# Performance work log

Measured on AMD Instinct MI355X. Metric: run time of the kernel, lower is better.

## Reference

```python
import jax, jax.numpy as jnp
import numpy as np

DIM = 256; WS = 8; HEADS = 8; HD = DIM // HEADS; SCALE = HD ** -0.5; MLP_HIDDEN = 1024
B = 8; H = 128; W = 128


def setup_inputs() -> dict:
    key = jax.random.key(0)
    ks = jax.random.split(key, 16)
    def nrm(k, shape, s=0.02):
        return jax.random.normal(k, shape, jnp.float32) * s
    # relative position index (same construction as torch buffer)
    coords = np.stack(np.meshgrid(np.arange(WS), np.arange(WS), indexing='ij')).reshape(2, -1)
    rel = (coords[:, :, None] - coords[:, None, :]).transpose(1, 2, 0).astype(np.int64)
    rel[..., 0] += WS - 1; rel[..., 1] += WS - 1; rel[..., 0] *= 2 * WS - 1
    rel_idx = jnp.asarray(rel.sum(-1), jnp.int32)  # (64,64) in [0,225)
    return dict(
        x=nrm(ks[0], (B, H, W, DIM), 1.0),
        rel_table=nrm(ks[1], ((2 * WS - 1) ** 2, HEADS)),
        qkv_w=nrm(ks[2], (3 * DIM, DIM)), qkv_b=nrm(ks[3], (3 * DIM,)),
        qkv2_w=nrm(ks[4], (3 * DIM, DIM)), qkv2_b=nrm(ks[5], (3 * DIM,)),
        proj_ln_w=jnp.ones((DIM,), jnp.float32), proj_ln_b=jnp.zeros((DIM,), jnp.float32),
        proj_w=nrm(ks[6], (DIM, DIM)), proj_b=nrm(ks[7], (DIM,)),
        proj2_ln_w=jnp.ones((DIM,), jnp.float32), proj2_ln_b=jnp.zeros((DIM,), jnp.float32),
        proj2_w=nrm(ks[8], (DIM, DIM)), proj2_b=nrm(ks[9], (DIM,)),
        norm1_w=jnp.ones((DIM,), jnp.float32), norm1_b=jnp.zeros((DIM,), jnp.float32),
        norm2_w=jnp.ones((DIM,), jnp.float32), norm2_b=jnp.zeros((DIM,), jnp.float32),
        fc1_w=nrm(ks[10], (MLP_HIDDEN, DIM)), fc1_b=nrm(ks[11], (MLP_HIDDEN,)),
        fc2_w=nrm(ks[12], (DIM, MLP_HIDDEN)), fc2_b=nrm(ks[13], (DIM,)),
        rel_idx=rel_idx,
    )


def _ln(x, w, b):
    mu = x.mean(-1, keepdims=True)
    var = ((x - mu) ** 2).mean(-1, keepdims=True)
    return (x - mu) / jnp.sqrt(var + 1e-5) * w + b


def _mha(tokens, wqkv, bqkv, bias=None):
    Bt, N, C = tokens.shape
    qkv = (tokens @ wqkv.T + bqkv).reshape(Bt, N, 3, HEADS, HD).transpose(2, 0, 3, 1, 4)
    q, k, v = qkv[0] * SCALE, qkv[1], qkv[2]
    attn = jnp.einsum('bhnd,bhmd->bhnm', q, k)
    if bias is not None:
        attn = attn + bias  # (1,heads,N,N) relative position bias
    attn = jax.nn.softmax(attn, axis=-1)
    out = jnp.einsum('bhnm,bhmd->bhnd', attn, v)
    return out.transpose(0, 2, 1, 3).reshape(Bt, N, C)


def _pos_sine(h, w, c):
    # PositionEmbeddingSine(normalize=True), mask all-zero -> cumsum = 1..h / 1..w
    npf = c // 2
    scale = 2.0 * np.pi; eps = 1e-5
    y = jnp.arange(1, h + 1, dtype=jnp.float32); y = y / (y[-1] + eps) * scale
    xw = jnp.arange(1, w + 1, dtype=jnp.float32); xw = xw / (xw[-1] + eps) * scale
    dim_t = 10000.0 ** ((2.0 * (jnp.arange(npf) // 2)) / npf)
    def enc(e):  # (L,) -> (L,npf) interleaved sin/cos
        p = e[:, None] / dim_t
        return jnp.stack([jnp.sin(p[:, 0::2]), jnp.cos(p[:, 1::2])], axis=-1).reshape(e.shape[0], npf)
    py = enc(y); px = enc(xw)
    return jnp.concatenate([jnp.broadcast_to(py[:, None, :], (h, w, npf)),
                            jnp.broadcast_to(px[None, :, :], (h, w, npf))], axis=-1)  # (h,w,c)


def _upsample_ac(x, oh, ow):
    # bilinear, align_corners=True; x: (B,h,w,C)
    Bn, h, w, C = x.shape
    def idx(n, o):
        s = jnp.linspace(0.0, n - 1.0, o)
        i0 = jnp.floor(s).astype(jnp.int32)
        i1 = jnp.minimum(i0 + 1, n - 1)
        return i0, i1, s - i0
    y0, y1, ty = idx(h, oh)
    x = x[:, y0] * (1 - ty)[None, :, None, None] + x[:, y1] * ty[None, :, None, None]
    x0, x1, tx = idx(w, ow)
    x = x[:, :, x0] * (1 - tx)[None, None, :, None] + x[:, :, x1] * tx[None, None, :, None]
    return x


def reference(x, rel_table, qkv_w, qkv_b, qkv2_w, qkv2_b,
              proj_ln_w, proj_ln_b, proj_w, proj_b,
              proj2_ln_w, proj2_ln_b, proj2_w, proj2_b,
              norm1_w, norm1_b, norm2_w, norm2_b,
              fc1_w, fc1_b, fc2_w, fc2_b, rel_idx):
    Bn, Hh, Ww, C = x.shape  # H,W divisible by WS -> padding is a no-op
    nh, nw = Hh // WS, Ww // WS
    N = WS * WS
    shortcut = x
    # window partition -> (B*nh*nw, N, C)
    xw = x.reshape(Bn, nh, WS, nw, WS, C).transpose(0, 1, 3, 2, 4, 5).reshape(-1, N, C)
    bias = rel_table[rel_idx.reshape(-1)].reshape(N, N, HEADS).transpose(2, 0, 1)[None]
    xw = _mha(xw, qkv_w, qkv_b, bias)
    xw = xw.reshape(Bn, nh, nw, WS, WS, C).transpose(0, 1, 3, 2, 4, 5).reshape(Bn, Hh, Ww, C)
    x = shortcut + xw
    x = x + (_ln(x, proj_ln_w, proj_ln_b) @ proj_w.T + proj_b)
    shortcut = x
    # global branch: avgpool each window, sine pos enc, full attention, bilinear upsample
    xg = x.reshape(Bn, nh, WS, nw, WS, C).mean(axis=(2, 4))  # (B,nh,nw,C)
    xg = xg + _pos_sine(nh, nw, C)[None]
    xg = _mha(xg.reshape(Bn, nh * nw, C), qkv2_w, qkv2_b).reshape(Bn, nh, nw, C)
    xg = _upsample_ac(xg, Hh, Ww)
    x = shortcut + xg
    x = x + (_ln(x, proj2_ln_w, proj2_ln_b) @ proj2_w.T + proj2_b)
    h = _ln(x, norm1_w, norm1_b)
    h = jax.nn.gelu(h @ fc1_w.T + fc1_b, approximate=False) @ fc2_w.T + fc2_b
    x = x + h
    return _ln(x, norm2_w, norm2_b)
```

## Files before the change

### kernel.cpp

```cpp
#include <hip/hip_runtime.h>
#include <math.h>

#define DEV __device__ __forceinline__

constexpr int NTOK = 131072;
constexpr int TOKS_PER_B = 16384;
constexpr float SCALE_F = 0.17677669529663687f;

typedef float f32x4 __attribute__((ext_vector_type(4)));
typedef _Float16 half8 __attribute__((ext_vector_type(8)));
typedef _Float16 half2v __attribute__((ext_vector_type(2)));
typedef unsigned short us8 __attribute__((ext_vector_type(8)));

#if defined(__has_builtin)
#if __has_builtin(__builtin_amdgcn_fdot2)
#define HAS_FDOT2 1
#endif
#endif

DEV float gelu1(float v) { return 0.5f * v * (1.f + erff(v * 0.7071067811865476f)); }
DEV unsigned short f2h(float x) { _Float16 h = (_Float16)x; return __builtin_bit_cast(unsigned short, h); }
DEV float h2f(unsigned short u) { return (float)__builtin_bit_cast(_Float16, u); }

DEV float dot2acc(unsigned qp, unsigned kp, float acc) {
#ifdef HAS_FDOT2
  return __builtin_amdgcn_fdot2(__builtin_bit_cast(half2v, qp),
                                __builtin_bit_cast(half2v, kp), acc, false);
#else
  return acc + h2f((unsigned short)(qp & 0xffff)) * h2f((unsigned short)(kp & 0xffff))
             + h2f((unsigned short)(qp >> 16)) * h2f((unsigned short)(kp >> 16));
#endif
}

DEV int swz_row(int p) { return ((p >> 2) & ~1) | (((p >> 2) ^ (p >> 4)) & 1); }
DEV int swz_gran(int p) {
  return ((p ^ (p >> 2) ^ (p >> 4)) & 1) | ((((p >> 1) ^ (p >> 3)) & 1) << 1);
}

#define GLOAD16(src, dst)                                                        \
  __builtin_amdgcn_global_load_lds(                                              \
      (const __attribute__((address_space(1))) void*)(src),                      \
      (__attribute__((address_space(3))) void*)(dst), 16, 0, 0)

__global__ void cvtw16_k(const float* __restrict__ w, unsigned short* __restrict__ dst, int n) {
  const int i = (blockIdx.x * 256 + threadIdx.x) * 4;
  float4 v = *(const float4*)(w + i);
  ushort4 h, l;
  h.x = f2h(v.x); l.x = f2h(v.x - h2f(h.x));
  h.y = f2h(v.y); l.y = f2h(v.y - h2f(h.y));
  h.z = f2h(v.z); l.z = f2h(v.z - h2f(h.z));
  h.w = f2h(v.w); l.w = f2h(v.w - h2f(h.w));
  *(ushort4*)(dst + i) = h;
  *(ushort4*)(dst + n + i) = l;
}

__global__ void biasprep_k(const float* __restrict__ rel_table, const int* __restrict__ rel_idx,
                           float* __restrict__ biasT) {
  const int i = blockIdx.x * 256 + threadIdx.x;
  const int h = i >> 12, mr = i & 4095, m = mr >> 6, r = mr & 63;
  biasT[i] = rel_table[rel_idx[r * 64 + m] * 8 + h];
}

template <int AMODE, bool RES, bool GELU, bool OUTH, bool STATS, bool FINLN>
__launch_bounds__(256)
__global__ void gemm16(const void* __restrict__ Ain, const unsigned short* __restrict__ Wp,
                       const float* __restrict__ bias, void* __restrict__ outv,
                       const float* __restrict__ stats,
                       const float* __restrict__ lnw, const float* __restrict__ lnb,
                       float* __restrict__ statsOut,
                       const float* __restrict__ fw, const float* __restrict__ fb,
                       int M, int N, int K) {
  __shared__ __align__(16) char Asm[64 * 64];
  __shared__ __align__(16) char Wsm[2 * 256 * 64];
  const int t = threadIdx.x;
  const int lane = t & 63, wid = t >> 6;
  const int m0 = blockIdx.y * 64, n0 = blockIdx.x * 256;
  const unsigned short* Wlp = Wp + (size_t)N * K;

  f32x4 acc[4][4];
#pragma unroll
  for (int i = 0; i < 4; ++i)
#pragma unroll
    for (int j = 0; j < 4; ++j) acc[i][j] = (f32x4){0.f, 0.f, 0.f, 0.f};

  const int fr = lane & 15, G = lane >> 4;
  const int sw16 = (((4 * fr + G) ^ (fr & 7)) << 4);

  const float* Afrow = nullptr;
  const unsigned short* Ahrow = nullptr;
  int aG = 0;
  float mu = 0.f, rsg = 1.f;
  if constexpr (AMODE == 2) {
    const int p = wid * 64 + lane;
    Ahrow = (const unsigned short*)Ain + (size_t)(m0 + swz_row(p)) * K + swz_gran(p) * 8;
  } else {
    const int p = t;
    const int aR = swz_row(p);
    aG = swz_gran(p);
    Afrow = (const float*)Ain + (size_t)(m0 + aR) * K + aG * 8;
    if constexpr (AMODE == 1) {
      mu = stats[(size_t)(m0 + aR) * 2];
      rsg = stats[(size_t)(m0 + aR) * 2 + 1];
    }
  }
  const unsigned short* wsrc[8];
  int wdst[8];
#pragma unroll
  for (int j = 0; j < 8; ++j) {
    const int plane = j >> 2;
    const int bs = (wid * 4 + (j & 3)) * 64;
    const int p = bs + lane;
    wsrc[j] = (plane ? Wlp : Wp) + (size_t)(n0 + swz_row(p)) * K + swz_gran(p) * 8;
    wdst[j] = plane * (256 * 64) + bs * 16;
  }

  for (int k0 = 0; k0 < K; k0 += 32) {
#pragma unroll
    for (int j = 0; j < 8; ++j) GLOAD16(wsrc[j] + k0, Wsm + wdst[j]);
    if constexpr (AMODE == 2) {
      GLOAD16(Ahrow + k0, Asm + wid * 1024);
    } else {
      float4 v0 = *(const float4*)(Afrow + k0);
      float4 v1 = *(const float4*)(Afrow + k0 + 4);
      if constexpr (AMODE == 1) {
        const int kc = k0 + aG * 8;
        float4 w0 = *(const float4*)(lnw + kc), w1 = *(const float4*)(lnw + kc + 4);
        float4 b0 = *(const float4*)(lnb + kc), b1 = *(const float4*)(lnb + kc + 4);
        v0.x = (v0.x - mu) * rsg * w0.x + b0.x;  v0.y = (v0.y - mu) * rsg * w0.y + b0.y;
        v0.z = (v0.z - mu) * rsg * w0.z + b0.z;  v0.w = (v0.w - mu) * rsg * w0.w + b0.w;
        v1.x = (v1.x - mu) * rsg * w1.x + b1.x;  v1.y = (v1.y - mu) * rsg * w1.y + b1.y;
        v1.z = (v1.z - mu) * rsg * w1.z + b1.z;  v1.w = (v1.w - mu) * rsg * w1.w + b1.w;
      }
      us8 hh;
      hh[0] = f2h(v0.x); hh[1] = f2h(v0.y); hh[2] = f2h(v0.z); hh[3] = f2h(v0.w);
      hh[4] = f2h(v1.x); hh[5] = f2h(v1.y); hh[6] = f2h(v1.z); hh[7] = f2h(v1.w);
      *(us8*)(Asm + t * 16) = hh;
    }
    __syncthreads();
    half8 a4[4], bh4[4], bl4[4];
#pragma unroll
    for (int i = 0; i < 4; ++i) {
      a4[i] = __builtin_bit_cast(half8, *(const us8*)(Asm + i * 1024 + sw16));
      bh4[i] = __builtin_bit_cast(half8, *(const us8*)(Wsm + wid * 4096 + i * 1024 + sw16));
      bl4[i] = __builtin_bit_cast(half8,
               *(const us8*)(Wsm + 256 * 64 + wid * 4096 + i * 1024 + sw16));
    }
#pragma unroll
    for (int i = 0; i < 4; ++i)
#pragma unroll
      for (int j = 0; j < 4; ++j) {
        acc[i][j] = __builtin_amdgcn_mfma_f32_16x16x32_f16(a4[i], bh4[j], acc[i][j], 0, 0, 0);
        acc[i][j] = __builtin_amdgcn_mfma_f32_16x16x32_f16(a4[i], bl4[j], acc[i][j], 0, 0, 0);
      }
    __syncthreads();
  }
  const int g4 = (lane >> 4) * 4;
#pragma unroll
  for (int i = 0; i < 4; ++i)
#pragma unroll
    for (int j = 0; j < 4; ++j) {
      const int col = n0 + wid * 64 + j * 16 + fr;
      const float bb = bias[col];
#pragma unroll
      for (int r4 = 0; r4 < 4; ++r4) {
        const int row = m0 + i * 16 + g4 + r4;
        float v = acc[i][j][r4] + bb;
        if (GELU) v = gelu1(v);
        if (RES) v += ((const float*)outv)[(size_t)row * N + col];
        acc[i][j][r4] = v;
      }
    }
  if (STATS || FINLN) {
    __shared__ float rsum[4][64], rsq[4][64];
    float ps[4][4], pq[4][4];
#pragma unroll
    for (int i = 0; i < 4; ++i)
#pragma unroll
      for (int r4 = 0; r4 < 4; ++r4) {
        ps[i][r4] = acc[i][0][r4] + acc[i][1][r4] + acc[i][2][r4] + acc[i][3][r4];
        pq[i][r4] = acc[i][0][r4] * acc[i][0][r4] + acc[i][1][r4] * acc[i][1][r4] +
                    acc[i][2][r4] * acc[i][2][r4] + acc[i][3][r4] * acc[i][3][r4];
      }
#pragma unroll
    for (int off = 1; off < 16; off <<= 1)
#pragma unroll
      for (int i = 0; i < 4; ++i)
#pragma unroll
        for (int r4 = 0; r4 < 4; ++r4) {
          ps[i][r4] += __shfl_xor(ps[i][r4], off, 64);
          pq[i][r4] += __shfl_xor(pq[i][r4], off, 64);
        }
    if (fr == 0) {
#pragma unroll
      for (int i = 0; i < 4; ++i)
#pragma unroll
        for (int r4 = 0; r4 < 4; ++r4) {
          rsum[wid][i * 16 + g4 + r4] = ps[i][r4];
          rsq[wid][i * 16 + g4 + r4] = pq[i][r4];
        }
    }
    __syncthreads();
#pragma unroll
    for (int i = 0; i < 4; ++i)
#pragma unroll
      for (int r4 = 0; r4 < 4; ++r4) {
        const int rl = i * 16 + g4 + r4;
        const float S = rsum[0][rl] + rsum[1][rl] + rsum[2][rl] + rsum[3][rl];
        const float Q = rsq[0][rl] + rsq[1][rl] + rsq[2][rl] + rsq[3][rl];
        const float mu2 = S * (1.f / 256.f);
        const float var = Q * (1.f / 256.f) - mu2 * mu2;
        const float rstd = 1.f / sqrtf(var + 1e-5f);
        if (STATS && wid == 0 && fr == 0) {
          statsOut[(size_t)(m0 + rl) * 2] = mu2;
          statsOut[(size_t)(m0 + rl) * 2 + 1] = rstd;
        }
        if (FINLN) {
#pragma unroll
          for (int j = 0; j < 4; ++j) {
            const int col = n0 + wid * 64 + j * 16 + fr;
            acc[i][j][r4] = (acc[i][j][r4] - mu2) * rstd * fw[col] + fb[col];
          }
        }
      }
  }
#pragma unroll
  for (int i = 0; i < 4; ++i)
#pragma unroll
    for (int j = 0; j < 4; ++j) {
      const int col = n0 + wid * 64 + j * 16 + fr;
#pragma unroll
      for (int r4 = 0; r4 < 4; ++r4) {
        const int row = m0 + i * 16 + g4 + r4;
        if (OUTH) ((unsigned short*)outv)[(size_t)row * N + col] = f2h(acc[i][j][r4]);
        else ((float*)outv)[(size_t)row * N + col] = acc[i][j][r4];
      }
    }
}

__launch_bounds__(64)
__global__ void winattn_k(const unsigned short* __restrict__ qkv, const float* __restrict__ xin,
                          float* __restrict__ X, const float* __restrict__ biasT, int b0) {
  __shared__ unsigned short klds[64][40];
  __shared__ float vlds[64][36];
  const int p = blockIdx.x;
  const int brel = p >> 11, rest = p & 2047;
  const int widx = rest >> 3, h = rest & 7;
  const int wy = widx >> 4, wx = widx & 15;
  const int r = threadIdx.x;
  const int tl = (wy * 8 + (r >> 3)) * 128 + wx * 8 + (r & 7);
  const unsigned short* qr = qkv + ((size_t)brel * TOKS_PER_B + tl) * 768 + h * 32;
  uint4 qa = __builtin_bit_cast(uint4, *(const us8*)(qr + 0));
  uint4 qb = __builtin_bit_cast(uint4, *(const us8*)(qr + 8));
  uint4 qc = __builtin_bit_cast(uint4, *(const us8*)(qr + 16));
  uint4 qd = __builtin_bit_cast(uint4, *(const us8*)(qr + 24));
#pragma unroll
  for (int jj = 0; jj < 4; ++jj)
    *(us8*)&klds[r][jj * 8] = *(const us8*)(qr + 256 + jj * 8);
#pragma unroll
  for (int jj = 0; jj < 4; ++jj) {
    us8 vv = *(const us8*)(qr + 512 + jj * 8);
    float4 f0, f1;
    f0.x = h2f(vv[0]); f0.y = h2f(vv[1]); f0.z = h2f(vv[2]); f0.w = h2f(vv[3]);
    f1.x = h2f(vv[4]); f1.y = h2f(vv[5]); f1.z = h2f(vv[6]); f1.w = h2f(vv[7]);
    *(float4*)&vlds[r][jj * 8] = f0;
    *(float4*)&vlds[r][jj * 8 + 4] = f1;
  }
  __syncthreads();

  const float* bf = biasT + h * 4096;
  float o[32];
#pragma unroll
  for (int e = 0; e < 32; ++e) o[e] = 0.f;
  float l = 0.f;
#pragma unroll 4
  for (int m = 0; m < 64; ++m) {
    uint4 k0 = *(const uint4*)&klds[m][0];
    uint4 k1 = *(const uint4*)&klds[m][8];
    uint4 k2 = *(const uint4*)&klds[m][16];
    uint4 k3 = *(const uint4*)&klds[m][24];
    float s = 0.f;
    s = dot2acc(qa.x, k0.x, s); s = dot2acc(qa.y, k0.y, s);
    s = dot2acc(qa.z, k0.z, s); s = dot2acc(qa.w, k0.w, s);
    s = dot2acc(qb.x, k1.x, s); s = dot2acc(qb.y, k1.y, s);
    s = dot2acc(qb.z, k1.z, s); s = dot2acc(qb.w, k1.w, s);
    s = dot2acc(qc.x, k2.x, s); s = dot2acc(qc.y, k2.y, s);
    s = dot2acc(qc.z, k2.z, s); s = dot2acc(qc.w, k2.w, s);
    s = dot2acc(qd.x, k3.x, s); s = dot2acc(qd.y, k3.y, s);
    s = dot2acc(qd.z, k3.z, s); s = dot2acc(qd.w, k3.w, s);
    const float pm = __expf(s * SCALE_F + bf[m * 64 + r]);
    l += pm;
    const float* vr = vlds[m];
#pragma unroll
    for (int e4 = 0; e4 < 8; ++e4) {
      float4 v4 = *(const float4*)(vr + e4 * 4);
      o[e4 * 4 + 0] += pm * v4.x; o[e4 * 4 + 1] += pm * v4.y;
      o[e4 * 4 + 2] += pm * v4.z; o[e4 * 4 + 3] += pm * v4.w;
    }
  }
  const float inv = 1.f / l;
  const size_t go = (size_t)((b0 + brel) * TOKS_PER_B + tl) * 256 + h * 32;
#pragma unroll
  for (int j4 = 0; j4 < 8; ++j4) {
    float4 xi = *(const float4*)(xin + go + j4 * 4);
    float4 rr;
    rr.x = o[j4*4+0] * inv + xi.x; rr.y = o[j4*4+1] * inv + xi.y;
    rr.z = o[j4*4+2] * inv + xi.z; rr.w = o[j4*4+3] * inv + xi.w;
    *(float4*)(X + go + j4 * 4) = rr;
  }
}

__global__ void lnstats_k(const float* __restrict__ X, float* __restrict__ stats) {
  const int lane = threadIdx.x & 63;
  const int wave = threadIdx.x >> 6;
  for (int tok = blockIdx.x * 4 + wave; tok < NTOK; tok += gridDim.x * 4) {
    float4 v = *(const float4*)(X + (size_t)tok * 256 + lane * 4);
    float s = v.x + v.y + v.z + v.w;
    float q = v.x*v.x + v.y*v.y + v.z*v.z + v.w*v.w;
#pragma unroll
    for (int off = 32; off > 0; off >>= 1) {
      s += __shfl_xor(s, off, 64);
      q += __shfl_xor(q, off, 64);
    }
    if (lane == 0) {
      const float m = s * (1.f / 256.f);
      const float var = q * (1.f / 256.f) - m * m;
      stats[(size_t)tok * 2] = m;
      stats[(size_t)tok * 2 + 1] = 1.f / sqrtf(var + 1e-5f);
    }
  }
}

__global__ void poolsine_k(const float* __restrict__ X, float* __restrict__ G0) {
  const int c = threadIdx.x;
  const int wx = blockIdx.x & 15, wy = (blockIdx.x >> 4) & 15, b = blockIdx.x >> 8;
  const float* base = X + ((size_t)(b * 128 + wy * 8) * 128 + wx * 8) * 256 + c;
  float s = 0.f;
  for (int ry = 0; ry < 8; ++ry)
#pragma unroll
    for (int rx = 0; rx < 8; ++rx) s += base[((size_t)ry * 128 + rx) * 256];
  s *= (1.f / 64.f);
  const float sc = 6.283185307179586f / (16.f + 1e-5f);
  const int cc = c & 127;
  const float d = powf(10000.f, (float)(cc >> 1) * (1.f / 64.f));
  const float e = ((c < 128 ? (float)(wy + 1) : (float)(wx + 1)) * sc) / d;
  const float pos = (cc & 1) ? cosf(e) : sinf(e);
  G0[(size_t)blockIdx.x * 256 + c] = s + pos;
}

__global__ void gattn_k(const float* __restrict__ G1, float* __restrict__ G2) {
  const int b = blockIdx.x, h = blockIdx.y, n = threadIdx.x;
  const float* qp = G1 + ((size_t)b * 256 + n) * 768 + h * 32;
  float q[32];
#pragma unroll
  for (int j4 = 0; j4 < 8; ++j4) {
    float4 v = *(const float4*)(qp + j4 * 4);
    q[j4*4+0] = v.x * SCALE_F; q[j4*4+1] = v.y * SCALE_F;
    q[j4*4+2] = v.z * SCALE_F; q[j4*4+3] = v.w * SCALE_F;
  }
  const float* kb = G1 + (size_t)b * 256 * 768 + 256 + h * 32;
  const float* vb = kb + 256;
  float out[32];
#pragma unroll
  for (int j = 0; j < 32; ++j) out[j] = 0.f;
  float mx = -3.4e38f, l = 0.f;
  for (int m = 0; m < 256; ++m) {
    const float* kr = kb + (size_t)m * 768;
    float s = 0.f;
#pragma unroll
    for (int j4 = 0; j4 < 8; ++j4) {
      float4 k4 = *(const float4*)(kr + j4 * 4);
      s += q[j4*4+0]*k4.x + q[j4*4+1]*k4.y + q[j4*4+2]*k4.z + q[j4*4+3]*k4.w;
    }
    const float mn = fmaxf(mx, s);
    const float corr = __expf(mx - mn);
    const float p = __expf(s - mn);
    l = l * corr + p;
    const float* vr = vb + (size_t)m * 768;
#pragma unroll
    for (int j4 = 0; j4 < 8; ++j4) {
      float4 v4 = *(const float4*)(vr + j4 * 4);
      out[j4*4+0] = out[j4*4+0]*corr + p*v4.x; out[j4*4+1] = out[j4*4+1]*corr + p*v4.y;
      out[j4*4+2] = out[j4*4+2]*corr + p*v4.z; out[j4*4+3] = out[j4*4+3]*corr + p*v4.w;
    }
    mx = mn;
  }
  const float inv = 1.f / l;
  float* op = G2 + ((size_t)b * 256 + n) * 256 + h * 32;
#pragma unroll
  for (int j4 = 0; j4 < 8; ++j4) {
    float4 r;
    r.x = out[j4*4+0]*inv; r.y = out[j4*4+1]*inv;
    r.z = out[j4*4+2]*inv; r.w = out[j4*4+3]*inv;
    *(float4*)(op + j4 * 4) = r;
  }
}

__global__ void upadd_k(float* __restrict__ X, const float* __restrict__ G2,
                        float* __restrict__ stats) {
  const int c = threadIdx.x;
  const int tok = blockIdx.x;
  const int j = tok & 127, i = (tok >> 7) & 127, b = tok >> 14;
  const float sy = i * (15.f / 127.f);
  const float sx = j * (15.f / 127.f);
  const int y0 = (int)sy; const float ty = sy - y0; const int y1 = min(y0 + 1, 15);
  const int x0 = (int)sx; const float tx = sx - x0; const int x1 = min(x0 + 1, 15);
  const float* gb = G2 + (size_t)b * 256 * 256;
  const float v00 = gb[((size_t)(y0 * 16 + x0)) * 256 + c];
  const float v01 = gb[((size_t)(y0 * 16 + x1)) * 256 + c];
  const float v10 = gb[((size_t)(y1 * 16 + x0)) * 256 + c];
  const float v11 = gb[((size_t)(y1 * 16 + x1)) * 256 + c];
  const float vy0 = v00 * (1.f - ty) + v10 * ty;
  const float vy1 = v01 * (1.f - ty) + v11 * ty;
  const float val = X[(size_t)tok * 256 + c] + vy0 * (1.f - tx) + vy1 * tx;
  X[(size_t)tok * 256 + c] = val;
  float s = val, q = val * val;
#pragma unroll
  for (int off = 32; off > 0; off >>= 1) {
    s += __shfl_xor(s, off, 64);
    q += __shfl_xor(q, off, 64);
  }
  __shared__ float red[8];
  const int lane = c & 63, wave = c >> 6;
  if (lane == 0) { red[wave * 2] = s; red[wave * 2 + 1] = q; }
  __syncthreads();
  if (c == 0) {
    const float S = red[0] + red[2] + red[4] + red[6];
    const float Q = red[1] + red[3] + red[5] + red[7];
    const float m = S * (1.f / 256.f);
    const float var = Q * (1.f / 256.f) - m * m;
    stats[(size_t)tok * 2] = m;
    stats[(size_t)tok * 2 + 1] = 1.f / sqrtf(var + 1e-5f);
  }
}

extern "C" void kernel_launch(void* const* d_in, const int* in_sizes, int n_in,
                              void* d_out, int out_size, void* d_ws, size_t ws_size,
                              hipStream_t stream) {
  const float* x          = (const float*)d_in[0];
  const float* rel_table  = (const float*)d_in[1];
  const float* qkv_w      = (const float*)d_in[2];
  const float* qkv_b      = (const float*)d_in[3];
  const float* qkv2_w     = (const float*)d_in[4];
  const float* qkv2_b     = (const float*)d_in[5];
  const float* proj_ln_w  = (const float*)d_in[6];
  const float* proj_ln_b  = (const float*)d_in[7];
  const float* proj_w     = (const float*)d_in[8];
  const float* proj_b     = (const float*)d_in[9];
  const float* proj2_ln_w = (const float*)d_in[10];
  const float* proj2_ln_b = (const float*)d_in[11];
  const float* proj2_w    = (const float*)d_in[12];
  const float* proj2_b    = (const float*)d_in[13];
  const float* norm1_w    = (const float*)d_in[14];
  const float* norm1_b    = (const float*)d_in[15];
  const float* norm2_w    = (const float*)d_in[16];
  const float* norm2_b    = (const float*)d_in[17];
  const float* fc1_w      = (const float*)d_in[18];
  const float* fc1_b      = (const float*)d_in[19];
  const float* fc2_w      = (const float*)d_in[20];
  const float* fc2_b      = (const float*)d_in[21];
  const int*   rel_idx    = (const int*)d_in[22];

  float* X = (float*)d_out;
  char* wsb = (char*)d_ws;
  float* stats = (float*)wsb;
  float* G0 = (float*)(wsb + (size_t)1048576);
  float* G1 = G0 + (size_t)2048 * 256;
  float* G2 = G1 + (size_t)2048 * 768;
  unsigned short* WCVT = (unsigned short*)(G2 + (size_t)2048 * 256);
  float* BIASF = (float*)((char*)WCVT + (size_t)4194304);
  char* BIG = (char*)BIASF + 131072;
  unsigned short* BIGH = (unsigned short*)BIG;
  const size_t fixed = (size_t)(BIG - wsb);
  const size_t avail = ws_size > fixed ? ws_size - fixed : 0;

  unsigned short* w_qkv  = WCVT;
  unsigned short* w_qkv2 = WCVT + 393216;
  unsigned short* w_proj = WCVT + 786432;
  unsigned short* w_proj2= WCVT + 917504;
  unsigned short* w_fc1  = WCVT + 1048576;
  unsigned short* w_fc2  = WCVT + 1572864;
  cvtw16_k<<<192, 256, 0, stream>>>(qkv_w,   w_qkv,   196608);
  cvtw16_k<<<192, 256, 0, stream>>>(qkv2_w,  w_qkv2,  196608);
  cvtw16_k<<<64,  256, 0, stream>>>(proj_w,  w_proj,   65536);
  cvtw16_k<<<64,  256, 0, stream>>>(proj2_w, w_proj2,  65536);
  cvtw16_k<<<256, 256, 0, stream>>>(fc1_w,   w_fc1,   262144);
  cvtw16_k<<<256, 256, 0, stream>>>(fc2_w,   w_fc2,   262144);
  biasprep_k<<<128, 256, 0, stream>>>(rel_table, rel_idx, BIASF);

  int st = 16384;
  if (avail >= (size_t)268435456) st = 131072;
  else if (avail >= (size_t)134217728) st = 65536;
  else if (avail >= (size_t)67108864) st = 32768;
  const bool one_shot = avail >= (size_t)NTOK * 768 * 2;

  if (one_shot) {
    gemm16<0, false, false, true, false, false><<<dim3(3, NTOK / 64), 256, 0, stream>>>(
        x, w_qkv, qkv_b, BIGH, nullptr, nullptr, nullptr, nullptr, nullptr, nullptr,
        NTOK, 768, 256);
    winattn_k<<<16384, 64, 0, stream>>>(BIGH, x, X, BIASF, 0);
  } else {
    for (int b = 0; b < 8; ++b) {
      gemm16<0, false, false, true, false, false><<<dim3(3, TOKS_PER_B / 64), 256, 0, stream>>>(
          x + (size_t)b * TOKS_PER_B * 256, w_qkv, qkv_b, BIGH,
          nullptr, nullptr, nullptr, nullptr, nullptr, nullptr, TOKS_PER_B, 768, 256);
      winattn_k<<<2048, 64, 0, stream>>>(BIGH, x, X, BIASF, b);
    }
  }
  lnstats_k<<<1024, 256, 0, stream>>>(X, stats);
  gemm16<1, true, false, false, false, false><<<dim3(1, NTOK / 64), 256, 0, stream>>>(
      X, w_proj, proj_b, X, stats, proj_ln_w, proj_ln_b, nullptr, nullptr, nullptr,
      NTOK, 256, 256);
  poolsine_k<<<2048, 256, 0, stream>>>(X, G0);
  gemm16<0, false, false, false, false, false><<<dim3(3, 32), 256, 0, stream>>>(
      G0, w_qkv2, qkv2_b, G1, nullptr, nullptr, nullptr, nullptr, nullptr, nullptr,
      2048, 768, 256);
  gattn_k<<<dim3(8, 8), 256, 0, stream>>>(G1, G2);
  upadd_k<<<NTOK, 256, 0, stream>>>(X, G2, stats);
  gemm16<1, true, false, false, true, false><<<dim3(1, NTOK / 64), 256, 0, stream>>>(
      X, w_proj2, proj2_b, X, stats, proj2_ln_w, proj2_ln_b, stats, nullptr, nullptr,
      NTOK, 256, 256);
  for (int s0 = 0; s0 < NTOK; s0 += st) {
    gemm16<1, false, true, true, false, false><<<dim3(4, st / 64), 256, 0, stream>>>(
        X + (size_t)s0 * 256, w_fc1, fc1_b, BIGH, stats + (size_t)s0 * 2,
        norm1_w, norm1_b, nullptr, nullptr, nullptr, st, 1024, 256);
    gemm16<2, true, false, false, false, true><<<dim3(1, st / 64), 256, 0, stream>>>(
        BIGH, w_fc2, fc2_b, X + (size_t)s0 * 256, nullptr, nullptr, nullptr, nullptr,
        norm2_w, norm2_b, st, 256, 1024);
  }
}
```

Before: 1.761 ms.

## Double-buffer GEMM shared-memory tiles and remap blocks for XCD-local L2 reuse

Turns the GEMM main loop into a two-stage pipeline. Shared-memory A and W tiles are double-buffered, and the next k-tile's global loads are issued before the current tile's MFMAs, which removes one barrier per iteration. It also remaps block indices so that consecutive blocks dispatched to the same XCD cover neighbouring M rows and share W tiles in L2. The cost is twice the LDS use (about 72KB per block), which may reduce occupancy, and extra registers held across the MFMA loop.

```diff
diff --git a/kernel.cpp b/kernel.cpp
--- a/kernel.cpp
+++ b/kernel.cpp
@@ -61,6 +61,27 @@
   biasT[i] = rel_table[rel_idx[r * 64 + m] * 8 + h];
 }
 
+#define STAGE_A_FINISH(BUFI, K0)                                                  \
+  do {                                                                            \
+    if constexpr (AMODE == 1) {                                                   \
+      const int kc = (K0) + aG * 8;                                               \
+      float4 w0 = *(const float4*)(lnw + kc), w1 = *(const float4*)(lnw + kc + 4);\
+      float4 b0 = *(const float4*)(lnb + kc), b1 = *(const float4*)(lnb + kc + 4);\
+      av0.x = (av0.x - mu) * rsg * w0.x + b0.x;                                   \
+      av0.y = (av0.y - mu) * rsg * w0.y + b0.y;                                   \
+      av0.z = (av0.z - mu) * rsg * w0.z + b0.z;                                   \
+      av0.w = (av0.w - mu) * rsg * w0.w + b0.w;                                   \
+      av1.x = (av1.x - mu) * rsg * w1.x + b1.x;                                   \
+      av1.y = (av1.y - mu) * rsg * w1.y + b1.y;                                   \
+      av1.z = (av1.z - mu) * rsg * w1.z + b1.z;                                   \
+      av1.w = (av1.w - mu) * rsg * w1.w + b1.w;                                   \
+    }                                                                             \
+    us8 hh;                                                                       \
+    hh[0] = f2h(av0.x); hh[1] = f2h(av0.y); hh[2] = f2h(av0.z); hh[3] = f2h(av0.w);\
+    hh[4] = f2h(av1.x); hh[5] = f2h(av1.y); hh[6] = f2h(av1.z); hh[7] = f2h(av1.w);\
+    *(us8*)(Asm[BUFI] + t * 16) = hh;                                             \
+  } while (0)
+
 template <int AMODE, bool RES, bool GELU, bool OUTH, bool STATS, bool FINLN>
 __launch_bounds__(256)
 __global__ void gemm16(const void* __restrict__ Ain, const unsigned short* __restrict__ Wp,
@@ -70,11 +91,21 @@
                        float* __restrict__ statsOut,
                        const float* __restrict__ fw, const float* __restrict__ fb,
                        int M, int N, int K) {
-  __shared__ __align__(16) char Asm[64 * 64];
-  __shared__ __align__(16) char Wsm[2 * 256 * 64];
+  __shared__ __align__(16) char Asm[2][4096];
+  __shared__ __align__(16) char Wsm[2][32768];
   const int t = threadIdx.x;
   const int lane = t & 63, wid = t >> 6;
-  const int m0 = blockIdx.y * 64, n0 = blockIdx.x * 256;
+  const int nx = gridDim.x, ny = gridDim.y;
+  const int d = blockIdx.x + nx * blockIdx.y;
+  int mb, nb;
+  if ((ny & 7) == 0) {
+    const int xcd = d & 7, j = d >> 3;
+    nb = j % nx;
+    mb = xcd * (ny >> 3) + j / nx;
+  } else {
+    nb = blockIdx.x; mb = blockIdx.y;
+  }
+  const int m0 = mb * 64, n0 = nb * 256;
   const unsigned short* Wlp = Wp + (size_t)N * K;
 
   f32x4 acc[4][4];
@@ -90,6 +121,7 @@
   const unsigned short* Ahrow = nullptr;
   int aG = 0;
   float mu = 0.f, rsg = 1.f;
+  float4 av0, av1;
   if constexpr (AMODE == 2) {
     const int p = wid * 64 + lane;
     Ahrow = (const unsigned short*)Ain + (size_t)(m0 + swz_row(p)) * K + swz_gran(p) * 8;
@@ -111,39 +143,43 @@
     const int bs = (wid * 4 + (j & 3)) * 64;
     const int p = bs + lane;
     wsrc[j] = (plane ? Wlp : Wp) + (size_t)(n0 + swz_row(p)) * K + swz_gran(p) * 8;
-    wdst[j] = plane * (256 * 64) + bs * 16;
-  }
-
-  for (int k0 = 0; k0 < K; k0 += 32) {
-#pragma unroll
-    for (int j = 0; j < 8; ++j) GLOAD16(wsrc[j] + k0, Wsm + wdst[j]);
-    if constexpr (AMODE == 2) {
-      GLOAD16(Ahrow + k0, Asm + wid * 1024);
-    } else {
-      float4 v0 = *(const float4*)(Afrow + k0);
-      float4 v1 = *(const float4*)(Afrow + k0 + 4);
-      if constexpr (AMODE == 1) {
-        const int kc = k0 + aG * 8;
-        float4 w0 = *(const float4*)(lnw + kc), w1 = *(const float4*)(lnw + kc + 4);
-        float4 b0 = *(const float4*)(lnb + kc), b1 = *(const float4*)(lnb + kc + 4);
-        v0.x = (v0.x - mu) * rsg * w0.x + b0.x;  v0.y = (v0.y - mu) * rsg * w0.y + b0.y;
-        v0.z = (v0.z - mu) * rsg * w0.z + b0.z;  v0.w = (v0.w - mu) * rsg * w0.w + b0.w;
-        v1.x = (v1.x - mu) * rsg * w1.x + b1.x;  v1.y = (v1.y - mu) * rsg * w1.y + b1.y;
-        v1.z = (v1.z - mu) * rsg * w1.z + b1.z;  v1.w = (v1.w - mu) * rsg * w1.w + b1.w;
+    wdst[j] = plane * 16384 + bs * 16;
+  }
+
+#pragma unroll
+  for (int j = 0; j < 8; ++j) GLOAD16(wsrc[j], Wsm[0] + wdst[j]);
+  if constexpr (AMODE == 2) {
+    GLOAD16(Ahrow, Asm[0] + wid * 1024);
+  } else {
+    av0 = *(const float4*)(Afrow);
+    av1 = *(const float4*)(Afrow + 4);
+    STAGE_A_FINISH(0, 0);
+  }
+  __syncthreads();
+
+  const int NT = K >> 5;
+  int buf = 0;
+  for (int tt = 0; tt < NT; ++tt) {
+    const int kn = (tt + 1) << 5;
+    const bool hasNext = (tt + 1) < NT;
+    if (hasNext) {
+#pragma unroll
+      for (int j = 0; j < 8; ++j) GLOAD16(wsrc[j] + kn, Wsm[buf ^ 1] + wdst[j]);
+      if constexpr (AMODE == 2) {
+        GLOAD16(Ahrow + kn, Asm[buf ^ 1] + wid * 1024);
+      } else {
+        av0 = *(const float4*)(Afrow + kn);
+        av1 = *(const float4*)(Afrow + kn + 4);
       }
-      us8 hh;
-      hh[0] = f2h(v0.x); hh[1] = f2h(v0.y); hh[2] = f2h(v0.z); hh[3] = f2h(v0.w);
-      hh[4] = f2h(v1.x); hh[5] = f2h(v1.y); hh[6] = f2h(v1.z); hh[7] = f2h(v1.w);
-      *(us8*)(Asm + t * 16) = hh;
-    }
-    __syncthreads();
+    }
     half8 a4[4], bh4[4], bl4[4];
 #pragma unroll
     for (int i = 0; i < 4; ++i) {
-      a4[i] = __builtin_bit_cast(half8, *(const us8*)(Asm + i * 1024 + sw16));
-      bh4[i] = __builtin_bit_cast(half8, *(const us8*)(Wsm + wid * 4096 + i * 1024 + sw16));
+      a4[i] = __builtin_bit_cast(half8, *(const us8*)(Asm[buf] + i * 1024 + sw16));
+      bh4[i] = __builtin_bit_cast(half8,
+               *(const us8*)(Wsm[buf] + wid * 4096 + i * 1024 + sw16));
       bl4[i] = __builtin_bit_cast(half8,
-               *(const us8*)(Wsm + 256 * 64 + wid * 4096 + i * 1024 + sw16));
+               *(const us8*)(Wsm[buf] + 16384 + wid * 4096 + i * 1024 + sw16));
     }
 #pragma unroll
     for (int i = 0; i < 4; ++i)
@@ -152,7 +188,11 @@
         acc[i][j] = __builtin_amdgcn_mfma_f32_16x16x32_f16(a4[i], bh4[j], acc[i][j], 0, 0, 0);
         acc[i][j] = __builtin_amdgcn_mfma_f32_16x16x32_f16(a4[i], bl4[j], acc[i][j], 0, 0, 0);
       }
-    __syncthreads();
+    if (hasNext) {
+      if constexpr (AMODE != 2) STAGE_A_FINISH(buf ^ 1, kn);
+      __syncthreads();
+    }
+    buf ^= 1;
   }
   const int g4 = (lane >> 4) * 4;
 #pragma unroll
@@ -170,7 +210,7 @@
         acc[i][j][r4] = v;
       }
     }
-  if (STATS || FINLN) {
+  if constexpr (STATS || FINLN) {
     __shared__ float rsum[4][64], rsq[4][64];
     float ps[4][4], pq[4][4];
 #pragma unroll
```

New measurement: 1.741 ms. Within noise of the previous version (-1.1%).
